# Optimization experiments

Measured on AMD Instinct MI355X. Metric: run time of the kernel, lower is better.

## Reference

```python
import jax, jax.numpy as jnp
import numpy as np

D = 128      # embedding_dim
E = 50000    # positive edges per metapath
S = 16       # negative samples per edge
N_A = 100000 # nodes of type A (head type of both metapaths)
N_B = 50000  # nodes of type B (tail type of metapath 1)


def setup_inputs() -> dict:
    key = jax.random.key(0)
    ks = jax.random.split(key, 10)
    emb_A = jax.random.normal(ks[0], (N_A, D), dtype=jnp.float32)
    emb_B = jax.random.normal(ks[1], (N_B, D), dtype=jnp.float32)
    # nn.init.uniform_(a=-1, b=1)
    rel_emb = jax.random.uniform(ks[2], (2, D, D), dtype=jnp.float32, minval=-1.0, maxval=1.0)
    edge_index_m0 = jax.random.randint(ks[3], (2, E), 0, N_A)  # A -> A
    edge_index_m1 = jnp.stack([
        jax.random.randint(ks[4], (E,), 0, N_A),               # heads: type A
        jax.random.randint(ks[5], (E,), 0, N_B),               # tails: type B
    ])
    neg_head_m0 = jax.random.randint(ks[6], (E, S), 0, N_A)
    neg_head_m1 = jax.random.randint(ks[7], (E, S), 0, N_A)
    neg_tail_m0 = jax.random.randint(ks[8], (E, S), 0, N_A)
    neg_tail_m1 = jax.random.randint(ks[9], (E, S), 0, N_B)
    return dict(emb_A=emb_A, emb_B=emb_B, rel_emb=rel_emb,
                edge_index_m0=edge_index_m0, edge_index_m1=edge_index_m1,
                neg_head_m0=neg_head_m0, neg_head_m1=neg_head_m1,
                neg_tail_m0=neg_tail_m0, neg_tail_m1=neg_tail_m1)


# The torch module computes score = (A K B^T).sum(dim=1); summing the [E,E]
# score matrix over dim 1 equals contracting with sum_j b_j, so we never
# materialize the [E,E] (or [E*S, E*S]) matrix -- same math, fused reduction.

def _pos_score(K, emb_h, emb_t, edge_index):
    s = emb_t[edge_index[1]].sum(0)          # [d] = sum_j b_j
    return emb_h[edge_index[0]] @ (K @ s)    # [E]


def _neg_head_score(K, emb_h, neg):
    # predict(mode='head'): emb_A = emb_h[neg.reshape(-1)],
    # idx_B = edge_index[0][arange(E)*S] == neg[:, 0],
    # side_B = (K @ emb_h[idx_B].T).repeat_interleave(S, -1); sum over columns
    # == K @ (S * sum_j emb_h[neg[j, 0]]).
    s = neg.shape[1]
    c = K @ (s * emb_h[neg[:, 0]].sum(0))    # [d]
    return emb_h[neg.reshape(-1)] @ c        # [E*S]


def _neg_tail_score(K, emb_t, neg):
    # predict(mode='tail'): emb_B = emb_t[neg.reshape(-1)],
    # idx_A = edge_index[1][arange(E)*S] == neg[:, 0],
    # side_A = (emb_t[idx_A] @ K).repeat_interleave(S, 0); row sums of
    # side_A @ emb_B^T == side_A @ sum_j emb_B[j].
    s = neg.shape[1]
    sb = emb_t[neg.reshape(-1)].sum(0)       # [d]
    base = (emb_t[neg[:, 0]] @ K) @ sb       # [E]
    return jnp.repeat(base, s)               # [E*S]


def reference(emb_A, emb_B, rel_emb, edge_index_m0, edge_index_m1,
              neg_head_m0, neg_head_m1, neg_tail_m0, neg_tail_m1):
    K0, K1 = rel_emb[0], rel_emb[1]
    pos0 = _pos_score(K0, emb_A, emb_A, edge_index_m0)   # [E]
    pos1 = _pos_score(K1, emb_A, emb_B, edge_index_m1)   # [E]
    nh0 = _neg_head_score(K0, emb_A, neg_head_m0)        # [E*S]
    nh1 = _neg_head_score(K1, emb_A, neg_head_m1)        # [E*S]
    nt0 = _neg_tail_score(K0, emb_A, neg_tail_m0)        # [E*S]
    nt1 = _neg_tail_score(K1, emb_B, neg_tail_m1)        # [E*S]
    return jnp.concatenate([pos0, pos1, nh0, nh1, nt0, nt1])
```

## Files before the change

### kernel.cpp

```cpp
#include <hip/hip_runtime.h>
#include <stdint.h>

#define D 128
#define E_EDGES 50000
#define S_NEG 16
#define N_A 100000
#define N_B 50000
#define ES (E_EDGES * S_NEG)

#define HW 12500
#define ACH 38
#define BCH 34

#define GA1 500
#define GB1 250
#define NCPY 16

#define S2_ROWS 128
#define GA2 ((N_A + S2_ROWS - 1) / S2_ROWS)
#define GB2 ((N_B + S2_ROWS - 1) / S2_ROWS)

__device__ inline float dot4(float4 a, float4 b) {
    return a.x * b.x + a.y * b.y + a.z * b.z + a.w * b.w;
}
__device__ inline void fma16(float* acc, const float4 w, const float4 x) {
    acc[0]  += w.x * x.x; acc[1]  += w.x * x.y; acc[2]  += w.x * x.z; acc[3]  += w.x * x.w;
    acc[4]  += w.y * x.x; acc[5]  += w.y * x.y; acc[6]  += w.y * x.z; acc[7]  += w.y * x.w;
    acc[8]  += w.z * x.x; acc[9]  += w.z * x.y; acc[10] += w.z * x.z; acc[11] += w.z * x.w;
    acc[12] += w.w * x.x; acc[13] += w.w * x.y; acc[14] += w.w * x.z; acc[15] += w.w * x.w;
}
__device__ inline void fma8(float* acc, const float2 w, const float4 x) {
    acc[0] += w.x * x.x; acc[1] += w.x * x.y; acc[2] += w.x * x.z; acc[3] += w.x * x.w;
    acc[4] += w.y * x.x; acc[5] += w.y * x.y; acc[6] += w.y * x.z; acc[7] += w.y * x.w;
}


__global__ void k_hist(const int* __restrict__ ei0, const int* __restrict__ ei1,
                       const int* __restrict__ nh0, const int* __restrict__ nh1,
                       const int* __restrict__ nt0, const int* __restrict__ nt1,
                       uint32_t* __restrict__ partA, uint32_t* __restrict__ partB,
                       float* __restrict__ svec) {
    __shared__ uint32_t h[HW];
    const int tid = threadIdx.x;
    if (blockIdx.x == 0) {
        for (int i = tid; i < NCPY * 6 * D; i += 512) svec[i] = 0.f;
    }
    for (int w = tid; w < HW; w += 512) h[w] = 0;
    __syncthreads();

    const int b = blockIdx.x;
    if (b < 2 * ACH) {
        const int c = b >> 1, hh = b & 1;
        const unsigned lo = hh * 50000u;
        uint32_t* dst = partA + (size_t)b * HW;
        if (c >= 2 && c < 6) {
            const int* src = (c < 4) ? nh0 : nh1;
            const long long base = (long long)(c & 1) * 25000 * S_NEG;
            for (int i = tid; i < 25000; i += 512) {
                const unsigned r = (unsigned)src[base + (long long)i * S_NEG] - lo;
                if (r < 50000u) atomicAdd(&h[r >> 2], 1u << ((r & 3u) * 8u));
            }
        } else {
            const int* srcp = (c < 2) ? (ei0 + E_EDGES + c * 25000)
                                      : (nt0 + (c - 6) * 25000);
            const int4* src4 = reinterpret_cast<const int4*>(srcp);
            for (int i = tid; i < 6250; i += 512) {
                const int4 v = src4[i];
                unsigned r;
                r = (unsigned)v.x - lo; if (r < 50000u) atomicAdd(&h[r >> 2], 1u << ((r & 3u) * 8u));
                r = (unsigned)v.y - lo; if (r < 50000u) atomicAdd(&h[r >> 2], 1u << ((r & 3u) * 8u));
                r = (unsigned)v.z - lo; if (r < 50000u) atomicAdd(&h[r >> 2], 1u << ((r & 3u) * 8u));
                r = (unsigned)v.w - lo; if (r < 50000u) atomicAdd(&h[r >> 2], 1u << ((r & 3u) * 8u));
            }
        }
        __syncthreads();
        for (int w = tid; w < HW; w += 512) dst[w] = h[w];
    } else {
        const int c = b - 2 * ACH;
        uint32_t* dst = partB + (size_t)c * HW;
        const int* srcp = (c < 2) ? (ei1 + E_EDGES + c * 25000)
                                  : (nt1 + (c - 2) * 25000);
        const int4* src4 = reinterpret_cast<const int4*>(srcp);
        for (int i = tid; i < 6250; i += 512) {
            const int4 v = src4[i];
            unsigned r;
            r = (unsigned)v.x; if (r < 50000u) atomicAdd(&h[r >> 2], 1u << ((r & 3u) * 8u));
            r = (unsigned)v.y; if (r < 50000u) atomicAdd(&h[r >> 2], 1u << ((r & 3u) * 8u));
            r = (unsigned)v.z; if (r < 50000u) atomicAdd(&h[r >> 2], 1u << ((r & 3u) * 8u));
            r = (unsigned)v.w; if (r < 50000u) atomicAdd(&h[r >> 2], 1u << ((r & 3u) * 8u));
        }
        __syncthreads();
        for (int w = tid; w < HW; w += 512) dst[w] = h[w];
    }
}

__global__ void __launch_bounds__(256, 4)
k_scan1(const float* __restrict__ embA, const float* __restrict__ embB,
        const uint32_t* __restrict__ partA, const uint32_t* __restrict__ partB,
        float* __restrict__ svec) {
    __shared__ float sds[4 * 512];
    __shared__ float4 cwbuf[200];
    const int tid = threadIdx.x;
    const int l = tid & 31;
    const int grp = tid >> 5;
    const int wid = tid >> 6;
    float* svdst = svec + (size_t)(blockIdx.x & (NCPY - 1)) * (6 * D);

    if ((int)blockIdx.x < GA1) {
        const int nb = blockIdx.x * 200;
        if (tid < 200) {
            const int n = nb + tid;
            const int hh = (n >= 50000);
            const int sh = (n & 3) * 8;
            const uint32_t* p = partA + (size_t)hh * HW + ((n - hh * 50000) >> 2);
            unsigned s0 = 0, s1 = 0, s2 = 0, s3 = 0;
#pragma unroll
            for (int c = 0; c < 2; ++c)  s0 += (p[(size_t)(c * 2) * HW] >> sh) & 255u;
#pragma unroll
            for (int c = 2; c < 4; ++c)  s1 += (p[(size_t)(c * 2) * HW] >> sh) & 255u;
#pragma unroll
            for (int c = 4; c < 6; ++c)  s2 += (p[(size_t)(c * 2) * HW] >> sh) & 255u;
#pragma unroll 8
            for (int c = 6; c < 38; ++c) s3 += (p[(size_t)(c * 2) * HW] >> sh) & 255u;
            cwbuf[tid] = make_float4((float)s0, (float)s1, (float)s2, (float)s3);
        }
        __syncthreads();

        const int r0 = nb + grp * 25;
        const int lr0 = grp * 25;
        const float* base = embA + 4 * l;
        float acc[16];
#pragma unroll
        for (int k = 0; k < 16; ++k) acc[k] = 0.f;
        float4 wc[5], xc[5];
#pragma unroll
        for (int u = 0; u < 5; ++u) {
            wc[u] = cwbuf[lr0 + u];
            xc[u] = *reinterpret_cast<const float4*>(base + (size_t)(r0 + u) * D);
        }
#pragma unroll
        for (int b = 0; b < 5; ++b) {
            float4 wn[5], xn[5];
            if (b < 4) {
#pragma unroll
                for (int u = 0; u < 5; ++u) {
                    const int rr = (b + 1) * 5 + u;
                    wn[u] = cwbuf[lr0 + rr];
                    xn[u] = *reinterpret_cast<const float4*>(base + (size_t)(r0 + rr) * D);
                }
            }
#pragma unroll
            for (int u = 0; u < 5; ++u) fma16(acc, wc[u], xc[u]);
            if (b < 4) {
#pragma unroll
                for (int u = 0; u < 5; ++u) { wc[u] = wn[u]; xc[u] = xn[u]; }
            }
        }
#pragma unroll
        for (int k = 0; k < 16; ++k) acc[k] += __shfl_xor(acc[k], 32);
        if ((tid & 32) == 0) {
            float* w0 = sds + wid * 512;
#pragma unroll
            for (int p = 0; p < 4; ++p)
                *reinterpret_cast<float4*>(w0 + p * 128 + 4 * l) =
                    make_float4(acc[4 * p], acc[4 * p + 1], acc[4 * p + 2], acc[4 * p + 3]);
        }
        __syncthreads();
        for (int j = tid; j < 512; j += 256)
            atomicAdd(&svdst[j], sds[j] + sds[512 + j] + sds[1024 + j] + sds[1536 + j]);
    } else {
        const int nb = (blockIdx.x - GA1) * 200;
        if (tid < 200) {
            const int n = nb + tid;
            const int sh = (n & 3) * 8;
            const uint32_t* p = partB + (n >> 2);
            unsigned s0 = 0, s1 = 0;
#pragma unroll
            for (int c = 0; c < 2; ++c)  s0 += (p[(size_t)c * HW] >> sh) & 255u;
#pragma unroll 8
            for (int c = 2; c < 34; ++c) s1 += (p[(size_t)c * HW] >> sh) & 255u;
            reinterpret_cast<float2*>(cwbuf)[tid] = make_float2((float)s0, (float)s1);
        }
        __syncthreads();
        const float2* cw2 = reinterpret_cast<const float2*>(cwbuf);

        const int r0 = nb + grp * 25;
        const int lr0 = grp * 25;
        const float* base = embB + 4 * l;
        float acc[8];
#pragma unroll
        for (int k = 0; k < 8; ++k) acc[k] = 0.f;
        float2 wc[5]; float4 xc[5];
#pragma unroll
        for (int u = 0; u < 5; ++u) {
            wc[u] = cw2[lr0 + u];
            xc[u] = *reinterpret_cast<const float4*>(base + (size_t)(r0 + u) * D);
        }
#pragma unroll
        for (int b = 0; b < 5; ++b) {
            float2 wn[5]; float4 xn[5];
            if (b < 4) {
#pragma unroll
                for (int u = 0; u < 5; ++u) {
                    const int rr = (b + 1) * 5 + u;
                    wn[u] = cw2[lr0 + rr];
                    xn[u] = *reinterpret_cast<const float4*>(base + (size_t)(r0 + rr) * D);
                }
            }
#pragma unroll
            for (int u = 0; u < 5; ++u) fma8(acc, wc[u], xc[u]);
            if (b < 4) {
#pragma unroll
                for (int u = 0; u < 5; ++u) { wc[u] = wn[u]; xc[u] = xn[u]; }
            }
        }
#pragma unroll
        for (int k = 0; k < 8; ++k) acc[k] += __shfl_xor(acc[k], 32);
        if ((tid & 32) == 0) {
            float* w0 = sds + wid * 256;
#pragma unroll
            for (int p = 0; p < 2; ++p)
                *reinterpret_cast<float4*>(w0 + p * 128 + 4 * l) =
                    make_float4(acc[4 * p], acc[4 * p + 1], acc[4 * p + 2], acc[4 * p + 3]);
        }
        __syncthreads();
        for (int j = tid; j < 256; j += 256)
            atomicAdd(&svdst[512 + j], sds[j] + sds[256 + j] + sds[512 + j] + sds[768 + j]);
    }
}

__global__ void k_cvec(const float* __restrict__ rel, const float* __restrict__ svec,
                       float* __restrict__ cvec) {
    __shared__ float sv[6 * D];
    const int tid = threadIdx.x;
    for (int e = tid; e < 6 * D; e += 256) {
        float s = 0.f;
#pragma unroll
        for (int c = 0; c < NCPY; ++c) s += svec[c * (6 * D) + e];
        sv[e] = s;
    }
    __syncthreads();
    for (int e = tid; e < 6 * D; e += 256) {
        const int j = e >> 7, i = e & 127;
        const int plane = (j == 0) ? 0 : (j == 1) ? 4 : (j == 5) ? 5 : (j - 1);
        const float4* Kp4 = reinterpret_cast<const float4*>(
            rel + (size_t)(j & 1) * (D * D) + (size_t)i * D);
        const float* s = sv + plane * D;
        float acc = 0.f;
#pragma unroll
        for (int k = 0; k < 32; ++k) {
            const float4 kk = Kp4[k];
            acc += kk.x * s[4 * k] + kk.y * s[4 * k + 1]
                 + kk.z * s[4 * k + 2] + kk.w * s[4 * k + 3];
        }
        cvec[j * D + i] = acc * ((j == 2 || j == 3) ? (float)S_NEG : 1.0f);
    }
}

__global__ void k_scan2(const float* __restrict__ embA, const float* __restrict__ embB,
                        const float* __restrict__ cvec,
                        float* __restrict__ PA, float* __restrict__ PB) {
    const int tid = threadIdx.x;
    const int sub = tid & 15;
    const int rloc = tid >> 4;

    if ((int)blockIdx.x < GA2) {
        float4 c0[5], c1[5];
#pragma unroll
        for (int j = 0; j < 5; ++j) {
            c0[j] = *reinterpret_cast<const float4*>(cvec + j * D + sub * 8);
            c1[j] = *reinterpret_cast<const float4*>(cvec + j * D + sub * 8 + 4);
        }
        const int base = blockIdx.x * S2_ROWS;
#pragma unroll 2
        for (int it = 0; it < S2_ROWS / 16; ++it) {
            const int row = base + it * 16 + rloc;
            const int rc = min(row, N_A - 1);
            const float* rp = embA + (size_t)rc * D + sub * 8;
            const float4 x0 = *reinterpret_cast<const float4*>(rp);
            const float4 x1 = *reinterpret_cast<const float4*>(rp + 4);
            float p0 = dot4(x0, c0[0]) + dot4(x1, c1[0]);
            float p1 = dot4(x0, c0[1]) + dot4(x1, c1[1]);
            float p2 = dot4(x0, c0[2]) + dot4(x1, c1[2]);
            float p3 = dot4(x0, c0[3]) + dot4(x1, c1[3]);
            float p4 = dot4(x0, c0[4]) + dot4(x1, c1[4]);
#pragma unroll
            for (int m = 1; m < 16; m <<= 1) {
                p0 += __shfl_xor(p0, m);
                p1 += __shfl_xor(p1, m);
                p2 += __shfl_xor(p2, m);
                p3 += __shfl_xor(p3, m);
                p4 += __shfl_xor(p4, m);
            }
            if (row < N_A) {
                if (sub == 0)      PA[row] = p0;
                else if (sub == 1) PA[(size_t)N_A + row] = p1;
                else if (sub == 2) PA[(size_t)2 * N_A + row] = p2;
                else if (sub == 3) PA[(size_t)3 * N_A + row] = p3;
                else if (sub == 4) PA[(size_t)4 * N_A + row] = p4;
            }
        }
    } else {
        const float4 c0 = *reinterpret_cast<const float4*>(cvec + 5 * D + sub * 8);
        const float4 c1 = *reinterpret_cast<const float4*>(cvec + 5 * D + sub * 8 + 4);
        const int base = (blockIdx.x - GA2) * S2_ROWS;
#pragma unroll 2
        for (int it = 0; it < S2_ROWS / 16; ++it) {
            const int row = base + it * 16 + rloc;
            const int rc = min(row, N_B - 1);
            const float* rp = embB + (size_t)rc * D + sub * 8;
            const float4 x0 = *reinterpret_cast<const float4*>(rp);
            const float4 x1 = *reinterpret_cast<const float4*>(rp + 4);
            float p = dot4(x0, c0) + dot4(x1, c1);
#pragma unroll
            for (int m = 1; m < 16; m <<= 1) p += __shfl_xor(p, m);
            if (row < N_B && sub == 0) PB[row] = p;
        }
    }
}

__global__ void k_scatter(const int* __restrict__ ei0, const int* __restrict__ ei1,
                          const int* __restrict__ nh0, const int* __restrict__ nh1,
                          const int* __restrict__ nt0, const int* __restrict__ nt1,
                          const float* __restrict__ PA, const float* __restrict__ PB,
                          float* __restrict__ out) {
    const int total4 = (2 * E_EDGES + 4 * ES) / 4;
    const float* P0 = PA;
    const float* P1 = PA + (size_t)N_A;
    const float* P2 = PA + (size_t)2 * N_A;
    const float* P3 = PA + (size_t)3 * N_A;
    const float* P4 = PA + (size_t)4 * N_A;
    for (int t = blockIdx.x * blockDim.x + threadIdx.x; t < total4;
         t += gridDim.x * blockDim.x) {
        const int e = t * 4;
        float4 v;
        if (e < E_EDGES) {
            const int4 i4 = *reinterpret_cast<const int4*>(ei0 + e);
            v = make_float4(P0[i4.x], P0[i4.y], P0[i4.z], P0[i4.w]);
        } else if (e < 2 * E_EDGES) {
            const int4 i4 = *reinterpret_cast<const int4*>(ei1 + (e - E_EDGES));
            v = make_float4(P1[i4.x], P1[i4.y], P1[i4.z], P1[i4.w]);
        } else if (e < 2 * E_EDGES + ES) {
            const int4 i4 = *reinterpret_cast<const int4*>(nh0 + (e - 2 * E_EDGES));
            v = make_float4(P2[i4.x], P2[i4.y], P2[i4.z], P2[i4.w]);
        } else if (e < 2 * E_EDGES + 2 * ES) {
            const int4 i4 = *reinterpret_cast<const int4*>(nh1 + (e - 2 * E_EDGES - ES));
            v = make_float4(P3[i4.x], P3[i4.y], P3[i4.z], P3[i4.w]);
        } else if (e < 2 * E_EDGES + 3 * ES) {
            const int i = e - 2 * E_EDGES - 2 * ES;
            const float s = P4[nt0[(i >> 4) << 4]];
            v = make_float4(s, s, s, s);
        } else {
            const int i = e - 2 * E_EDGES - 3 * ES;
            const float s = PB[nt1[(i >> 4) << 4]];
            v = make_float4(s, s, s, s);
        }
        *reinterpret_cast<float4*>(out + e) = v;
    }
}

extern "C" void kernel_launch(void* const* d_in, const int* in_sizes, int n_in,
                              void* d_out, int out_size, void* d_ws, size_t ws_size,
                              hipStream_t stream) {
    const float* embA = (const float*)d_in[0];
    const float* embB = (const float*)d_in[1];
    const float* rel  = (const float*)d_in[2];
    const int* ei0 = (const int*)d_in[3];
    const int* ei1 = (const int*)d_in[4];
    const int* nh0 = (const int*)d_in[5];
    const int* nh1 = (const int*)d_in[6];
    const int* nt0 = (const int*)d_in[7];
    const int* nt1 = (const int*)d_in[8];
    float* out = (float*)d_out;

    uint32_t* partA = (uint32_t*)d_ws;
    uint32_t* partB = partA + (size_t)2 * ACH * HW;
    float* svec = (float*)(partB + (size_t)BCH * HW);
    float* cvec = svec + (size_t)NCPY * 6 * D;
    float* PA   = cvec + 6 * D;
    float* PB   = PA + (size_t)5 * N_A;

    k_hist<<<2 * ACH + BCH, 512, 0, stream>>>(ei0, ei1, nh0, nh1, nt0, nt1,
                                              partA, partB, svec);
    k_scan1<<<GA1 + GB1, 256, 0, stream>>>(embA, embB, partA, partB, svec);
    k_cvec<<<1, 256, 0, stream>>>(rel, svec, cvec);
    k_scan2<<<GA2 + GB2, 256, 0, stream>>>(embA, embB, cvec, PA, PB);
    k_scatter<<<2048, 256, 0, stream>>>(ei0, ei1, nh0, nh1, nt0, nt1, PA, PB, out);
}
```

Baseline: 192.1 us.

## Replace LDS partial histograms with global float atomic count arrays

The per-block shared-memory byte-packed histograms, which were written to many partial buffers and then reduced in the scan kernel, are replaced by direct global float atomicAdd into per-node interleaved count arrays (4 slots per A node, 2 per B node). A separate zero kernel clears the counts and svec, and the scan kernel now reads a single float4/float2 per node instead of summing dozens of partial words. This removes the partial-buffer write/read traffic and the reduction loop. In exchange it adds about 1.7M global atomics with possible contention and an extra kernel launch.

```diff
diff --git a/kernel.cpp b/kernel.cpp
--- a/kernel.cpp
+++ b/kernel.cpp
@@ -8,10 +8,6 @@
 #define N_B 50000
 #define ES (E_EDGES * S_NEG)
 
-#define HW 12500
-#define ACH 38
-#define BCH 34
-
 #define GA1 500
 #define GB1 250
 #define NCPY 16
@@ -19,6 +15,11 @@
 #define S2_ROWS 128
 #define GA2 ((N_A + S2_ROWS - 1) / S2_ROWS)
 #define GB2 ((N_B + S2_ROWS - 1) / S2_ROWS)
+
+#define NT_U 200000
+#define EIT_U 12500
+#define FLAT_U (2 * NT_U + 2 * EIT_U)
+#define ZERO_F4 ((4 * N_A + 2 * N_B + NCPY * 6 * D) / 4)
 
 __device__ inline float dot4(float4 a, float4 b) {
     return a.x * b.x + a.y * b.y + a.z * b.z + a.w * b.w;
@@ -35,68 +36,48 @@
 }
 
 
+__global__ void k_zero(float4* __restrict__ dst) {
+    const int nth = gridDim.x * blockDim.x;
+    for (int u = blockIdx.x * blockDim.x + threadIdx.x; u < ZERO_F4; u += nth)
+        dst[u] = make_float4(0.f, 0.f, 0.f, 0.f);
+}
+
 __global__ void k_hist(const int* __restrict__ ei0, const int* __restrict__ ei1,
                        const int* __restrict__ nh0, const int* __restrict__ nh1,
                        const int* __restrict__ nt0, const int* __restrict__ nt1,
-                       uint32_t* __restrict__ partA, uint32_t* __restrict__ partB,
-                       float* __restrict__ svec) {
-    __shared__ uint32_t h[HW];
-    const int tid = threadIdx.x;
-    if (blockIdx.x == 0) {
-        for (int i = tid; i < NCPY * 6 * D; i += 512) svec[i] = 0.f;
-    }
-    for (int w = tid; w < HW; w += 512) h[w] = 0;
-    __syncthreads();
-
-    const int b = blockIdx.x;
-    if (b < 2 * ACH) {
-        const int c = b >> 1, hh = b & 1;
-        const unsigned lo = hh * 50000u;
-        uint32_t* dst = partA + (size_t)b * HW;
-        if (c >= 2 && c < 6) {
-            const int* src = (c < 4) ? nh0 : nh1;
-            const long long base = (long long)(c & 1) * 25000 * S_NEG;
-            for (int i = tid; i < 25000; i += 512) {
-                const unsigned r = (unsigned)src[base + (long long)i * S_NEG] - lo;
-                if (r < 50000u) atomicAdd(&h[r >> 2], 1u << ((r & 3u) * 8u));
-            }
+                       float* __restrict__ cntA, float* __restrict__ cntB) {
+    const int t0 = blockIdx.x * blockDim.x + threadIdx.x;
+    const int nth = gridDim.x * blockDim.x;
+
+    for (int u = t0; u < FLAT_U; u += nth) {
+        int4 v; float* b; int s, o;
+        if (u < NT_U) {
+            v = reinterpret_cast<const int4*>(nt0)[u];            b = cntA; s = 4; o = 3;
+        } else if (u < 2 * NT_U) {
+            v = reinterpret_cast<const int4*>(nt1)[u - NT_U];     b = cntB; s = 2; o = 1;
+        } else if (u < 2 * NT_U + EIT_U) {
+            v = reinterpret_cast<const int4*>(ei0 + E_EDGES)[u - 2 * NT_U];
+            b = cntA; s = 4; o = 0;
         } else {
-            const int* srcp = (c < 2) ? (ei0 + E_EDGES + c * 25000)
-                                      : (nt0 + (c - 6) * 25000);
-            const int4* src4 = reinterpret_cast<const int4*>(srcp);
-            for (int i = tid; i < 6250; i += 512) {
-                const int4 v = src4[i];
-                unsigned r;
-                r = (unsigned)v.x - lo; if (r < 50000u) atomicAdd(&h[r >> 2], 1u << ((r & 3u) * 8u));
-                r = (unsigned)v.y - lo; if (r < 50000u) atomicAdd(&h[r >> 2], 1u << ((r & 3u) * 8u));
-                r = (unsigned)v.z - lo; if (r < 50000u) atomicAdd(&h[r >> 2], 1u << ((r & 3u) * 8u));
-                r = (unsigned)v.w - lo; if (r < 50000u) atomicAdd(&h[r >> 2], 1u << ((r & 3u) * 8u));
-            }
-        }
-        __syncthreads();
-        for (int w = tid; w < HW; w += 512) dst[w] = h[w];
-    } else {
-        const int c = b - 2 * ACH;
-        uint32_t* dst = partB + (size_t)c * HW;
-        const int* srcp = (c < 2) ? (ei1 + E_EDGES + c * 25000)
-                                  : (nt1 + (c - 2) * 25000);
-        const int4* src4 = reinterpret_cast<const int4*>(srcp);
-        for (int i = tid; i < 6250; i += 512) {
-            const int4 v = src4[i];
-            unsigned r;
-            r = (unsigned)v.x; if (r < 50000u) atomicAdd(&h[r >> 2], 1u << ((r & 3u) * 8u));
-            r = (unsigned)v.y; if (r < 50000u) atomicAdd(&h[r >> 2], 1u << ((r & 3u) * 8u));
-            r = (unsigned)v.z; if (r < 50000u) atomicAdd(&h[r >> 2], 1u << ((r & 3u) * 8u));
-            r = (unsigned)v.w; if (r < 50000u) atomicAdd(&h[r >> 2], 1u << ((r & 3u) * 8u));
-        }
-        __syncthreads();
-        for (int w = tid; w < HW; w += 512) dst[w] = h[w];
+            v = reinterpret_cast<const int4*>(ei1 + E_EDGES)[u - 2 * NT_U - EIT_U];
+            b = cntB; s = 2; o = 0;
+        }
+        atomicAdd(b + (size_t)v.x * s + o, 1.f);
+        atomicAdd(b + (size_t)v.y * s + o, 1.f);
+        atomicAdd(b + (size_t)v.z * s + o, 1.f);
+        atomicAdd(b + (size_t)v.w * s + o, 1.f);
+    }
+    for (int u = t0; u < 2 * E_EDGES; u += nth) {
+        if (u < E_EDGES)
+            atomicAdd(&cntA[4 * (size_t)nh0[(size_t)u * S_NEG] + 1], 1.f);
+        else
+            atomicAdd(&cntA[4 * (size_t)nh1[(size_t)(u - E_EDGES) * S_NEG] + 2], 1.f);
     }
 }
 
 __global__ void __launch_bounds__(256, 4)
 k_scan1(const float* __restrict__ embA, const float* __restrict__ embB,
-        const uint32_t* __restrict__ partA, const uint32_t* __restrict__ partB,
+        const float* __restrict__ cntA, const float* __restrict__ cntB,
         float* __restrict__ svec) {
     __shared__ float sds[4 * 512];
     __shared__ float4 cwbuf[200];
@@ -108,22 +89,8 @@
 
     if ((int)blockIdx.x < GA1) {
         const int nb = blockIdx.x * 200;
-        if (tid < 200) {
-            const int n = nb + tid;
-            const int hh = (n >= 50000);
-            const int sh = (n & 3) * 8;
-            const uint32_t* p = partA + (size_t)hh * HW + ((n - hh * 50000) >> 2);
-            unsigned s0 = 0, s1 = 0, s2 = 0, s3 = 0;
-#pragma unroll
-            for (int c = 0; c < 2; ++c)  s0 += (p[(size_t)(c * 2) * HW] >> sh) & 255u;
-#pragma unroll
-            for (int c = 2; c < 4; ++c)  s1 += (p[(size_t)(c * 2) * HW] >> sh) & 255u;
-#pragma unroll
-            for (int c = 4; c < 6; ++c)  s2 += (p[(size_t)(c * 2) * HW] >> sh) & 255u;
-#pragma unroll 8
-            for (int c = 6; c < 38; ++c) s3 += (p[(size_t)(c * 2) * HW] >> sh) & 255u;
-            cwbuf[tid] = make_float4((float)s0, (float)s1, (float)s2, (float)s3);
-        }
+        if (tid < 200)
+            cwbuf[tid] = reinterpret_cast<const float4*>(cntA)[nb + tid];
         __syncthreads();
 
         const int r0 = nb + grp * 25;
@@ -170,17 +137,9 @@
             atomicAdd(&svdst[j], sds[j] + sds[512 + j] + sds[1024 + j] + sds[1536 + j]);
     } else {
         const int nb = (blockIdx.x - GA1) * 200;
-        if (tid < 200) {
-            const int n = nb + tid;
-            const int sh = (n & 3) * 8;
-            const uint32_t* p = partB + (n >> 2);
-            unsigned s0 = 0, s1 = 0;
-#pragma unroll
-            for (int c = 0; c < 2; ++c)  s0 += (p[(size_t)c * HW] >> sh) & 255u;
-#pragma unroll 8
-            for (int c = 2; c < 34; ++c) s1 += (p[(size_t)c * HW] >> sh) & 255u;
-            reinterpret_cast<float2*>(cwbuf)[tid] = make_float2((float)s0, (float)s1);
-        }
+        if (tid < 200)
+            reinterpret_cast<float2*>(cwbuf)[tid] =
+                reinterpret_cast<const float2*>(cntB)[nb + tid];
         __syncthreads();
         const float2* cw2 = reinterpret_cast<const float2*>(cwbuf);
 
@@ -373,16 +332,16 @@
     const int* nt1 = (const int*)d_in[8];
     float* out = (float*)d_out;
 
-    uint32_t* partA = (uint32_t*)d_ws;
-    uint32_t* partB = partA + (size_t)2 * ACH * HW;
-    float* svec = (float*)(partB + (size_t)BCH * HW);
+    float* cntA = (float*)d_ws;
+    float* cntB = cntA + (size_t)4 * N_A;
+    float* svec = cntB + (size_t)2 * N_B;
     float* cvec = svec + (size_t)NCPY * 6 * D;
     float* PA   = cvec + 6 * D;
     float* PB   = PA + (size_t)5 * N_A;
 
-    k_hist<<<2 * ACH + BCH, 512, 0, stream>>>(ei0, ei1, nh0, nh1, nt0, nt1,
-                                              partA, partB, svec);
-    k_scan1<<<GA1 + GB1, 256, 0, stream>>>(embA, embB, partA, partB, svec);
+    k_zero<<<64, 256, 0, stream>>>((float4*)d_ws);
+    k_hist<<<512, 256, 0, stream>>>(ei0, ei1, nh0, nh1, nt0, nt1, cntA, cntB);
+    k_scan1<<<GA1 + GB1, 256, 0, stream>>>(embA, embB, cntA, cntB, svec);
     k_cvec<<<1, 256, 0, stream>>>(rel, svec, cvec);
     k_scan2<<<GA2 + GB2, 256, 0, stream>>>(embA, embB, cvec, PA, PB);
     k_scatter<<<2048, 256, 0, stream>>>(ei0, ei1, nh0, nh1, nt0, nt1, PA, PB, out);
```

Measured after the change: 257.9 us. +34.3%, slower.
